# Kernel tuning notes

Hardware: AMD Instinct MI355X
Metric: run time of the kernel (lower is better)

## Reference

```python
import jax, jax.numpy as jnp
import numpy as np

B, C, L, K = 8, 128, 32768, 129  # batch, seq_len (channels), samples, filter length


def setup_inputs() -> dict:
    key = jax.random.key(0)
    k0, k1, k2, k3 = jax.random.split(key, 4)
    return {
        "x": jax.random.normal(k0, (B, C, L), dtype=jnp.float32),
        "weights_mag": jnp.ones((C, 1), dtype=jnp.float32),
        "weights_angle": jax.random.uniform(k1, (C, 1), dtype=jnp.float32),
        "kernel_real": jax.random.normal(k2, (K,), dtype=jnp.float32),
        "kernel_imag": jax.random.normal(k3, (K,), dtype=jnp.float32),
    }


def _matched_filter(x, kr, ki):
    # PyTorch F.conv1d is cross-correlation; mf_coeffs = conj(kernel) repeated per
    # channel (groups = C), so every channel is correlated with the SAME conj kernel.
    # Input is real (x.to(complex64) has zero imag), so:
    #   out = corr(x, conj(k)) = corr(x, kr) - 1j * corr(x, ki)
    b, c, l = x.shape
    kk = kr.shape[0]
    pad = kk // 2
    w = jnp.stack([kr, -ki])[:, None, :]  # [2, 1, K]: real and imag of conj kernel
    y = jax.lax.conv_general_dilated(
        x.reshape(b * c, 1, l), w,
        window_strides=(1,), padding=[(pad, pad)],
        dimension_numbers=("NCH", "OIH", "NCH"),
    )  # [B*C, 2, L]
    yr = y[:, 0].reshape(b, c, l)
    yi = y[:, 1].reshape(b, c, l)
    return yr + 1j * yi  # complex64


def reference(x, weights_mag, weights_angle, kernel_real, kernel_imag):
    batch = x.shape[0]
    y = _matched_filter(x, kernel_real, kernel_imag)          # [B, C, L] complex64
    phase = jnp.arctan(weights_angle)                          # [C, 1]
    norm_mag = batch * jax.nn.softmax(weights_mag, axis=0)     # [C, 1]
    scale = (norm_mag.astype(jnp.complex64) * jnp.exp(-1j * phase))  # [C, 1] complex
    return scale * y
```

## Files before the change

### kernel.cpp

```cpp
#include <hip/hip_runtime.h>
#include <hip/hip_bf16.h>
#include <math.h>

constexpr int Bc = 8, Cc = 128, Lc = 32768, Kc = 129, PAD = Kc / 2;

constexpr int ROWS   = 16;
constexpr int MLEN   = 1024;
constexpr int PSPAN  = MLEN + 144;
constexpr int PSTR   = 1176;
constexpr int THREADS= 512;
constexpr int NTILES = MLEN / 16;
constexpr int NWAVES = THREADS / 64;
constexpr int TPW    = NTILES / NWAVES;

typedef __attribute__((ext_vector_type(8))) short short8;
typedef __attribute__((ext_vector_type(4))) float floatx4;

__device__ __forceinline__ unsigned short f2bf(float f) {
    unsigned u = __builtin_bit_cast(unsigned, f);
    u += 0x7fffu + ((u >> 16) & 1u);
    return (unsigned short)(u >> 16);
}

__global__ void scale_kernel(const float* __restrict__ wm,
                             const float* __restrict__ wa,
                             float* __restrict__ ws, int C, float batchf) {
    int c = threadIdx.x;
    if (c >= C) return;
    float m = -1e30f;
    for (int i = 0; i < C; ++i) m = fmaxf(m, wm[i]);
    float s = 0.f;
    for (int i = 0; i < C; ++i) s += expf(wm[i] - m);
    float nm = batchf * expf(wm[c] - m) / s;
    float a = wa[c];
    float inv = rsqrtf(1.f + a * a);
    ws[2 * c]     = nm * inv;
    ws[2 * c + 1] = nm * a * inv;
}

__global__ __launch_bounds__(THREADS)
void mf_kernel(const float* __restrict__ x,
               const float* __restrict__ kr,
               const float* __restrict__ ki,
               const float* __restrict__ sc_ss,
               float* __restrict__ out, int interleaved) {
    __shared__ __align__(16) unsigned short lx[ROWS * PSTR];

    const int bx   = blockIdx.x;
    const int bg   = blockIdx.y;
    const int row0 = bg * ROWS;
    const int P0   = bx * MLEN;
    const int s0   = P0 - PAD;

    const int tid  = threadIdx.x;
    const int lane = tid & 63;
    const int fh   = lane >> 4;
    const int fn   = lane & 15;

    short8 ar[5], ai[5];
    #pragma unroll
    for (int d = 0; d < 5; ++d) {
        #pragma unroll
        for (int e = 0; e < 8; ++e) {
            int idx = 32 * d + 8 * fh + e - fn;
            bool ok = (idx >= 0) && (idx < Kc);
            ar[d][e] = (short)f2bf(ok ? kr[idx] : 0.f);
            ai[d][e] = (short)f2bf(ok ? ki[idx] : 0.f);
        }
    }

    const int srow = tid >> 5;
    const int scol = tid & 31;
    const float* __restrict__ xr = x + (size_t)(row0 + srow) * Lc;
    unsigned short* lrow = &lx[srow * PSTR];
    const bool interior = (s0 >= 0) && (s0 + PSPAN <= Lc);
    for (int i4 = scol; i4 < PSPAN / 4; i4 += 32) {
        int g = s0 + 4 * i4;
        float4 v;
        if (interior) {
            v = *reinterpret_cast<const float4*>(xr + g);
        } else {
            v.x = (g + 0 >= 0 && g + 0 < Lc) ? xr[g + 0] : 0.f;
            v.y = (g + 1 >= 0 && g + 1 < Lc) ? xr[g + 1] : 0.f;
            v.z = (g + 2 >= 0 && g + 2 < Lc) ? xr[g + 2] : 0.f;
            v.w = (g + 3 >= 0 && g + 3 < Lc) ? xr[g + 3] : 0.f;
        }
        ushort4 h;
        h.x = f2bf(v.x); h.y = f2bf(v.y); h.z = f2bf(v.z); h.w = f2bf(v.w);
        *reinterpret_cast<ushort4*>(&lrow[4 * i4]) = h;
    }
    __syncthreads();

    const int ch = (row0 + fn) & (Cc - 1);
    const float scv = sc_ss[2 * ch];
    const float ssv = sc_ss[2 * ch + 1];
    const int wv = tid >> 6;

    for (int jj = 0; jj < TPW; ++jj) {
        const int j  = wv * TPW + jj;
        const int pb = 16 * j;
        const unsigned short* lp = &lx[fn * PSTR + pb + 8 * fh];
        floatx4 cr = {0.f, 0.f, 0.f, 0.f};
        floatx4 cim = {0.f, 0.f, 0.f, 0.f};
        #pragma unroll
        for (int d = 0; d < 5; ++d) {
            short8 b = *reinterpret_cast<const short8*>(lp + 32 * d);
            cr  = __builtin_amdgcn_mfma_f32_16x16x32_bf16(ar[d], b, cr, 0, 0, 0);
            cim = __builtin_amdgcn_mfma_f32_16x16x32_bf16(ai[d], b, cim, 0, 0, 0);
        }
        const size_t obase = (size_t)(row0 + fn) * Lc + P0 + pb + 4 * fh;
        if (!interleaved) {
            float4 o;
            o.x = scv * cr[0] - ssv * cim[0];
            o.y = scv * cr[1] - ssv * cim[1];
            o.z = scv * cr[2] - ssv * cim[2];
            o.w = scv * cr[3] - ssv * cim[3];
            *reinterpret_cast<float4*>(out + obase) = o;
        } else {
            float2* o2 = reinterpret_cast<float2*>(out) + obase;
            #pragma unroll
            for (int r = 0; r < 4; ++r) {
                o2[r] = make_float2(scv * cr[r] - ssv * cim[r],
                                    -scv * cim[r] - ssv * cr[r]);
            }
        }
    }
}

extern "C" void kernel_launch(void* const* d_in, const int* in_sizes, int n_in,
                              void* d_out, int out_size, void* d_ws, size_t ws_size,
                              hipStream_t stream) {
    const float* x  = (const float*)d_in[0];
    const float* wm = (const float*)d_in[1];
    const float* wa = (const float*)d_in[2];
    const float* kr = (const float*)d_in[3];
    const float* ki = (const float*)d_in[4];
    float* out = (float*)d_out;
    float* ws  = (float*)d_ws;

    const int C = in_sizes[1];
    const long long N = (long long)Bc * Cc * Lc;
    const int interleaved = (out_size == 2 * N) ? 1 : 0;

    hipLaunchKernelGGL(scale_kernel, dim3(1), dim3(C), 0, stream,
                       wm, wa, ws, C, (float)Bc);

    dim3 grid(Lc / MLEN, (Bc * Cc) / ROWS);
    hipLaunchKernelGGL(mf_kernel, grid, dim3(THREADS), 0, stream,
                       x, kr, ki, ws, out, interleaved);
}
```

Measured before the change: 83.33 us.

## Process four chunks per block with double-buffered LDS and register prefetch

After: 118.2 us. +41.9%, slower.

```diff
diff --git a/kernel.cpp b/kernel.cpp
--- a/kernel.cpp
+++ b/kernel.cpp
@@ -6,20 +6,21 @@
 
 constexpr int ROWS   = 16;
 constexpr int MLEN   = 1024;
+constexpr int NCHUNK = 4;
 constexpr int PSPAN  = MLEN + 144;
 constexpr int PSTR   = 1176;
 constexpr int THREADS= 512;
 constexpr int NTILES = MLEN / 16;
 constexpr int NWAVES = THREADS / 64;
 constexpr int TPW    = NTILES / NWAVES;
+constexpr int NF     = 10;
+constexpr int NQ     = PSPAN / 4;
 
 typedef __attribute__((ext_vector_type(8))) short short8;
 typedef __attribute__((ext_vector_type(4))) float floatx4;
 
 __device__ __forceinline__ unsigned short f2bf(float f) {
-    unsigned u = __builtin_bit_cast(unsigned, f);
-    u += 0x7fffu + ((u >> 16) & 1u);
-    return (unsigned short)(u >> 16);
+    return __builtin_bit_cast(unsigned short, __float2bfloat16(f));
 }
 
 __global__ void scale_kernel(const float* __restrict__ wm,
@@ -38,24 +39,23 @@
     ws[2 * c + 1] = nm * a * inv;
 }
 
-__global__ __launch_bounds__(THREADS)
+__global__ __launch_bounds__(THREADS, 4)
 void mf_kernel(const float* __restrict__ x,
                const float* __restrict__ kr,
                const float* __restrict__ ki,
                const float* __restrict__ sc_ss,
                float* __restrict__ out, int interleaved) {
-    __shared__ __align__(16) unsigned short lx[ROWS * PSTR];
+    __shared__ __align__(16) unsigned short lx[2][ROWS * PSTR];
 
     const int bx   = blockIdx.x;
     const int bg   = blockIdx.y;
     const int row0 = bg * ROWS;
-    const int P0   = bx * MLEN;
-    const int s0   = P0 - PAD;
 
     const int tid  = threadIdx.x;
     const int lane = tid & 63;
     const int fh   = lane >> 4;
     const int fn   = lane & 15;
+    const int wv   = tid >> 6;
 
     short8 ar[5], ai[5];
     #pragma unroll
@@ -69,61 +69,98 @@
         }
     }
 
+    const int ch = (row0 + fn) & (Cc - 1);
+    const float scv = sc_ss[2 * ch];
+    const float ssv = sc_ss[2 * ch + 1];
+
     const int srow = tid >> 5;
     const int scol = tid & 31;
     const float* __restrict__ xr = x + (size_t)(row0 + srow) * Lc;
-    unsigned short* lrow = &lx[srow * PSTR];
-    const bool interior = (s0 >= 0) && (s0 + PSPAN <= Lc);
-    for (int i4 = scol; i4 < PSPAN / 4; i4 += 32) {
-        int g = s0 + 4 * i4;
-        float4 v;
-        if (interior) {
-            v = *reinterpret_cast<const float4*>(xr + g);
-        } else {
-            v.x = (g + 0 >= 0 && g + 0 < Lc) ? xr[g + 0] : 0.f;
-            v.y = (g + 1 >= 0 && g + 1 < Lc) ? xr[g + 1] : 0.f;
-            v.z = (g + 2 >= 0 && g + 2 < Lc) ? xr[g + 2] : 0.f;
-            v.w = (g + 3 >= 0 && g + 3 < Lc) ? xr[g + 3] : 0.f;
+
+    auto LOADCHUNK = [&](int gc, float4* v) {
+        const int s0 = gc * MLEN - PAD;
+        const bool interior = (s0 >= 0) && (s0 + PSPAN <= Lc);
+        #pragma unroll
+        for (int i = 0; i < NF; ++i) {
+            const int i4 = scol + 32 * i;
+            if (i4 < NQ) {
+                const int g = s0 + 4 * i4;
+                if (interior) {
+                    v[i] = *reinterpret_cast<const float4*>(xr + g);
+                } else {
+                    v[i].x = (g + 0 >= 0 && g + 0 < Lc) ? xr[g + 0] : 0.f;
+                    v[i].y = (g + 1 >= 0 && g + 1 < Lc) ? xr[g + 1] : 0.f;
+                    v[i].z = (g + 2 >= 0 && g + 2 < Lc) ? xr[g + 2] : 0.f;
+                    v[i].w = (g + 3 >= 0 && g + 3 < Lc) ? xr[g + 3] : 0.f;
+                }
+            }
         }
-        ushort4 h;
-        h.x = f2bf(v.x); h.y = f2bf(v.y); h.z = f2bf(v.z); h.w = f2bf(v.w);
-        *reinterpret_cast<ushort4*>(&lrow[4 * i4]) = h;
-    }
+    };
+
+    auto WRITECHUNK = [&](int buf, const float4* v) {
+        unsigned short* lrow = &lx[buf][srow * PSTR];
+        #pragma unroll
+        for (int i = 0; i < NF; ++i) {
+            const int i4 = scol + 32 * i;
+            if (i4 < NQ) {
+                __hip_bfloat162 p0 = __float22bfloat162_rn(make_float2(v[i].x, v[i].y));
+                __hip_bfloat162 p1 = __float22bfloat162_rn(make_float2(v[i].z, v[i].w));
+                ushort2 u0, u1;
+                __builtin_memcpy(&u0, &p0, 4);
+                __builtin_memcpy(&u1, &p1, 4);
+                ushort4 h;
+                h.x = u0.x; h.y = u0.y; h.z = u1.x; h.w = u1.y;
+                *reinterpret_cast<ushort4*>(&lrow[4 * i4]) = h;
+            }
+        }
+    };
+
+    auto COMPUTE = [&](int buf, int P0) {
+        #pragma unroll
+        for (int jj = 0; jj < TPW; ++jj) {
+            const int j  = wv * TPW + jj;
+            const int pb = 16 * j;
+            const unsigned short* lp = &lx[buf][fn * PSTR + pb + 8 * fh];
+            floatx4 cr = {0.f, 0.f, 0.f, 0.f};
+            floatx4 cim = {0.f, 0.f, 0.f, 0.f};
+            #pragma unroll
+            for (int d = 0; d < 5; ++d) {
+                short8 b = *reinterpret_cast<const short8*>(lp + 32 * d);
+                cr  = __builtin_amdgcn_mfma_f32_16x16x32_bf16(ar[d], b, cr, 0, 0, 0);
+                cim = __builtin_amdgcn_mfma_f32_16x16x32_bf16(ai[d], b, cim, 0, 0, 0);
+            }
+            const size_t obase = (size_t)(row0 + fn) * Lc + P0 + pb + 4 * fh;
+            if (!interleaved) {
+                floatx4 o;
+                o[0] = scv * cr[0] - ssv * cim[0];
+                o[1] = scv * cr[1] - ssv * cim[1];
+                o[2] = scv * cr[2] - ssv * cim[2];
+                o[3] = scv * cr[3] - ssv * cim[3];
+                __builtin_nontemporal_store(o, reinterpret_cast<floatx4*>(out + obase));
+            } else {
+                float2* o2 = reinterpret_cast<float2*>(out) + obase;
+                #pragma unroll
+                for (int r = 0; r < 4; ++r) {
+                    o2[r] = make_float2(scv * cr[r] - ssv * cim[r],
+                                        -scv * cim[r] - ssv * cr[r]);
+                }
+            }
+        }
+    };
+
+    const int gc0 = bx * NCHUNK;
+    float4 v[NF];
+    LOADCHUNK(gc0, v);
+    WRITECHUNK(0, v);
     __syncthreads();
 
-    const int ch = (row0 + fn) & (Cc - 1);
-    const float scv = sc_ss[2 * ch];
-    const float ssv = sc_ss[2 * ch + 1];
-    const int wv = tid >> 6;
-
-    for (int jj = 0; jj < TPW; ++jj) {
-        const int j  = wv * TPW + jj;
-        const int pb = 16 * j;
-        const unsigned short* lp = &lx[fn * PSTR + pb + 8 * fh];
-        floatx4 cr = {0.f, 0.f, 0.f, 0.f};
-        floatx4 cim = {0.f, 0.f, 0.f, 0.f};
-        #pragma unroll
-        for (int d = 0; d < 5; ++d) {
-            short8 b = *reinterpret_cast<const short8*>(lp + 32 * d);
-            cr  = __builtin_amdgcn_mfma_f32_16x16x32_bf16(ar[d], b, cr, 0, 0, 0);
-            cim = __builtin_amdgcn_mfma_f32_16x16x32_bf16(ai[d], b, cim, 0, 0, 0);
-        }
-        const size_t obase = (size_t)(row0 + fn) * Lc + P0 + pb + 4 * fh;
-        if (!interleaved) {
-            float4 o;
-            o.x = scv * cr[0] - ssv * cim[0];
-            o.y = scv * cr[1] - ssv * cim[1];
-            o.z = scv * cr[2] - ssv * cim[2];
-            o.w = scv * cr[3] - ssv * cim[3];
-            *reinterpret_cast<float4*>(out + obase) = o;
-        } else {
-            float2* o2 = reinterpret_cast<float2*>(out) + obase;
-            #pragma unroll
-            for (int r = 0; r < 4; ++r) {
-                o2[r] = make_float2(scv * cr[r] - ssv * cim[r],
-                                    -scv * cim[r] - ssv * cr[r]);
-            }
-        }
+    #pragma unroll
+    for (int c = 0; c < NCHUNK; ++c) {
+        float4 vn[NF];
+        if (c + 1 < NCHUNK) LOADCHUNK(gc0 + c + 1, vn);
+        COMPUTE(c & 1, (gc0 + c) * MLEN);
+        if (c + 1 < NCHUNK) WRITECHUNK((c + 1) & 1, vn);
+        __syncthreads();
     }
 }
 
@@ -145,7 +182,7 @@
     hipLaunchKernelGGL(scale_kernel, dim3(1), dim3(C), 0, stream,
                        wm, wa, ws, C, (float)Bc);
 
-    dim3 grid(Lc / MLEN, (Bc * Cc) / ROWS);
+    dim3 grid(Lc / (MLEN * NCHUNK), (Bc * Cc) / ROWS);
     hipLaunchKernelGGL(mf_kernel, grid, dim3(THREADS), 0, stream,
                        x, kr, ki, ws, out, interleaved);
 }
```
